# Kernel tuning notes

Hardware: AMD Instinct MI355X
Metric: run time of the kernel (lower is better)

The kernel has to match this reference:

```python
import jax, jax.numpy as jnp
import numpy as np

NA, NV, FEAT = 8000, 4000, 32
H, D = 4, 16            # heads, per-head dim
HD = H * D              # 64 node width
BLOCKS, DEPTH = 6, 2    # 12 attention layers total
OUT = 64
AK, AVK, VK = 10, 15, 15
EPS = 1e-5


def setup_inputs() -> dict:
    key = jax.random.key(0)
    ks = jax.random.split(key, 16)
    rn = lambda k, s, sc=0.1: (jax.random.normal(k, s, dtype=jnp.float32) * sc)
    return {
        "atom_x": rn(ks[0], (NA, FEAT), 1.0),
        "atom_pos": rn(ks[1], (NA, 3), 1.0),
        "vox_x": rn(ks[2], (NV, FEAT), 1.0),
        "vox_pos": rn(ks[3], (NV, 3), 1.0),
        "W_atom_in": rn(ks[4], (FEAT, HD)),
        "b_atom_in": jnp.zeros((HD,), jnp.float32),
        "W_vox_in": rn(ks[5], (FEAT, HD)),
        "b_vox_in": jnp.zeros((HD,), jnp.float32),
        "emlp_w1": rn(ks[6], (3, 1, 8), 0.5),
        "emlp_b1": jnp.zeros((3, 8), jnp.float32),
        "emlp_w2": rn(ks[7], (3, 8, 1), 0.5),
        "emlp_b2": jnp.zeros((3, 1), jnp.float32),
        "ln_g": jnp.ones((BLOCKS * DEPTH, HD), jnp.float32),
        "ln_b": jnp.zeros((BLOCKS * DEPTH, HD), jnp.float32),
        "Ws": rn(ks[8], (BLOCKS * DEPTH, HD, HD)),
        "Wd": rn(ks[9], (BLOCKS * DEPTH, HD, HD)),
        "We": rn(ks[10], (BLOCKS * DEPTH, 1, HD)),
        "att": rn(ks[11], (BLOCKS * DEPTH, H, D)),
        "Wo1": rn(ks[12], ((BLOCKS + 1) * HD, HD)),
        "bo1": jnp.zeros((HD,), jnp.float32),
        "Wo2": rn(ks[13], (HD, OUT)),
        "bo2": jnp.zeros((OUT,), jnp.float32),
    }


def _knn_edges(q_pos, c_pos, k, q_off, c_off):
    # for each query, k nearest candidates (single-graph batch)
    d2 = (jnp.sum(q_pos * q_pos, 1, keepdims=True)
          - 2.0 * q_pos @ c_pos.T
          + jnp.sum(c_pos * c_pos, 1))                      # [Nq, Nc]
    idx = jax.lax.top_k(-d2, k)[1]                          # [Nq, k]
    src = (idx + c_off).reshape(-1)
    dst = jnp.repeat(jnp.arange(q_pos.shape[0]) + q_off, k)
    return src, dst


def _forward(atom_x, atom_pos, vox_x, vox_pos,
             W_atom_in, b_atom_in, W_vox_in, b_vox_in,
             emlp_w1, emlp_b1, emlp_w2, emlp_b2,
             ln_g, ln_b, Ws, Wd, We, att, Wo1, bo1, Wo2, bo2):
    Na, Nv = atom_x.shape[0], vox_x.shape[0]
    N = Na + Nv
    x = jnp.concatenate([atom_x @ W_atom_in + b_atom_in,
                         vox_x @ W_vox_in + b_vox_in], 0)   # [N, HD]
    pos = jnp.concatenate([atom_pos, vox_pos], 0)           # [N, 3]

    # (query_pos, cand_pos, k, q_offset, c_offset, edge-MLP index)
    combos = [(atom_pos, atom_pos, AK, 0, 0, 0),    # atom<-atom
              (atom_pos, vox_pos, AVK, 0, Na, 1),   # atom<-vox
              (vox_pos, vox_pos, VK, Na, Na, 2)]    # vox<-vox
    srcs, dsts, attrs = [], [], []
    for qp, cp, k, qo, co, mi in combos:
        s, d = _knn_edges(qp, cp, k, qo, co)
        dist = jnp.linalg.norm(pos[s] - pos[d], axis=1, keepdims=True)  # [E,1]
        h = jax.nn.relu(dist @ emlp_w1[mi] + emlp_b1[mi])
        attrs.append(h @ emlp_w2[mi] + emlp_b2[mi])
        srcs.append(s); dsts.append(d)
    src = jnp.concatenate(srcs)
    dst = jnp.concatenate(dsts)
    eattr = jnp.concatenate(attrs, 0)                       # [E,1]

    def gat_layer(xin, l):
        mu = xin.mean(-1, keepdims=True)
        var = xin.var(-1, keepdims=True)
        h = (xin - mu) * jax.lax.rsqrt(var + EPS) * ln_g[l] + ln_b[l]
        s = (h @ Ws[l]).reshape(N, H, D)
        d_ = (h @ Wd[l]).reshape(N, H, D)
        e = (eattr @ We[l]).reshape(-1, H, D)
        m = s[src] + d_[dst] + e                            # [E,H,D]
        score = jnp.einsum('ehd,hd->eh', jax.nn.leaky_relu(m, 0.2), att[l])
        smax = jax.ops.segment_max(score, dst, num_segments=N)
        a = jnp.exp(score - smax[dst])
        denom = jax.ops.segment_sum(a, dst, num_segments=N)
        alpha = a / denom[dst]                              # softmax per dst node
        msg = jax.ops.segment_sum(alpha[..., None] * s[src], dst,
                                  num_segments=N).reshape(N, HD)
        return jax.nn.relu(xin + msg)

    outs = [x]
    cur = x
    for b in range(BLOCKS):
        for dd in range(DEPTH):
            cur = gat_layer(cur, b * DEPTH + dd)
        outs.append(cur)
    cat = jnp.concatenate(outs, -1)[Na:]                    # vox nodes, [Nv,448]
    enc = jax.nn.relu(cat @ Wo1 + bo1) @ Wo2 + bo2          # [Nv,OUT]
    return enc


def reference(atom_x, atom_pos, vox_x, vox_pos,
              W_atom_in, b_atom_in, W_vox_in, b_vox_in,
              emlp_w1, emlp_b1, emlp_w2, emlp_b2,
              ln_g, ln_b, Ws, Wd, We, att, Wo1, bo1, Wo2, bo2):
    enc = _forward(atom_x, atom_pos, vox_x, vox_pos,
                   W_atom_in, b_atom_in, W_vox_in, b_vox_in,
                   emlp_w1, emlp_b1, emlp_w2, emlp_b2,
                   ln_g, ln_b, Ws, Wd, We, att, Wo1, bo1, Wo2, bo2)
    return (enc, vox_pos)
```

## Files before the change

kernel.cpp:

```cpp
#include <hip/hip_runtime.h>
#include <math.h>

#define NA 8000
#define NV 4000
#define NN 12000
#define NA_PAD 8192
#define NV_PAD 4096
#define KNN_TILE 2048
#define FEAT 32
#define HD 64
#define NLAYER 12
#define E_AA 80000
#define E_AV 120000
#define E_VV 60000
#define E_TOT 260000
#define ENC_SIZE (NV * HD)
#define EPS 1e-5f

__device__ __forceinline__ float wave_sum64(float v) {
#pragma unroll
  for (int off = 1; off < 64; off <<= 1) v += __shfl_xor(v, off);
  return v;
}

__device__ __forceinline__ float dpp_step(float v, const int ctrl) {
  int p;
  switch (ctrl) {
    case 0xB1:  p = __builtin_amdgcn_update_dpp(0, __float_as_int(v), 0xB1,  0xF, 0xF, true); break;
    case 0x4E:  p = __builtin_amdgcn_update_dpp(0, __float_as_int(v), 0x4E,  0xF, 0xF, true); break;
    case 0x141: p = __builtin_amdgcn_update_dpp(0, __float_as_int(v), 0x141, 0xF, 0xF, true); break;
    default:    p = __builtin_amdgcn_update_dpp(0, __float_as_int(v), 0x140, 0xF, 0xF, true); break;
  }
  return v + __int_as_float(p);
}

__device__ __forceinline__ float head_sum16_dpp(float v) {
  v = dpp_step(v, 0xB1);
  v = dpp_step(v, 0x4E);
  v = dpp_step(v, 0x141);
  v = dpp_step(v, 0x140);
  return v;
}

__device__ __forceinline__ float wave_sum64_dpp(float v) {
  v = head_sum16_dpp(v);
  v += __shfl_xor(v, 16);
  v += __shfl_xor(v, 32);
  return v;
}

__global__ __launch_bounds__(256) void pack_kernel(
    const float* __restrict__ apos, const float* __restrict__ vpos,
    float4* __restrict__ apk, float4* __restrict__ vpk)
{
  const int i = blockIdx.x * 256 + threadIdx.x;
  if (i < NA_PAD) {
    float4 r;
    if (i < NA) {
      const float cx = apos[i*3+0], cy = apos[i*3+1], cz = apos[i*3+2];
      r = make_float4(cx, cy, cz, (cx*cx + cy*cy) + cz*cz);
    } else r = make_float4(0.f, 0.f, 0.f, INFINITY);
    apk[i] = r;
  } else {
    const int j = i - NA_PAD;
    if (j < NV_PAD) {
      float4 r;
      if (j < NV) {
        const float cx = vpos[j*3+0], cy = vpos[j*3+1], cz = vpos[j*3+2];
        r = make_float4(cx, cy, cz, (cx*cx + cy*cy) + cz*cz);
      } else r = make_float4(0.f, 0.f, 0.f, INFINITY);
      vpk[j] = r;
    }
  }
}

template<int K, int NC_PAD>
__device__ __attribute__((noinline)) void knn_body(
    const float* __restrict__ qpos, const float4* __restrict__ cpk,
    int c_off, int* __restrict__ out_src, int qblock)
{
  extern __shared__ float4 tile[];
  const int tid  = threadIdx.x;
  const int wid  = tid >> 6, lane = tid & 63;
  const int q    = qblock * 8 + wid;
  const float qx = qpos[q*3+0], qy = qpos[q*3+1], qz = qpos[q*3+2];
  const float qq = (qx*qx + qy*qy) + qz*qz;

  float eD = INFINITY; int eI = 0x7fffffff;
  float thrD = INFINITY;

  for (int t0 = 0; t0 < NC_PAD; t0 += KNN_TILE) {
    __syncthreads();
#pragma unroll
    for (int s = 0; s < KNN_TILE/512; ++s)
      tile[s*512 + tid] = cpk[t0 + s*512 + tid];
    __syncthreads();
#pragma unroll 8
    for (int it = 0; it < KNN_TILE/64; ++it) {
      const int j = t0 + it*64 + lane;
      const float4 c = tile[it*64 + lane];
      const float dot = qx*c.x + qy*c.y + qz*c.z;
      const float d2  = (qq - 2.0f*dot) + c.w;
      unsigned long long m = __ballot(d2 < thrD);
      if (m) {
        do {
          const int sl = __ffsll(m) - 1;
          m &= (m - 1ULL);
          const float v  = __shfl(d2, sl);
          const int   vi = j - lane + sl;
          const bool stay = (eD < v) || (eD == v && eI < vi);
          const float pD = __shfl_up(eD, 1);
          const int   pI = __shfl_up(eI, 1);
          int pS = __shfl_up(stay ? 1 : 0, 1);
          if (lane == 0) pS = 1;
          eD = stay ? eD : (pS ? v  : pD);
          eI = stay ? eI : (pS ? vi : pI);
        } while (m);
        thrD = __shfl(eD, K-1);
      }
    }
  }
  if (lane < K) out_src[q*K + lane] = eI + c_off;
}

__global__ __launch_bounds__(512) void knn_all_kernel(
    const float* __restrict__ apos, const float* __restrict__ vpos,
    const float4* __restrict__ apk, const float4* __restrict__ vpk,
    int* __restrict__ srcA, int* __restrict__ srcAV, int* __restrict__ srcVV)
{
  const int b = blockIdx.x;
  if (b < NA/8)
    knn_body<10, NA_PAD>(apos, apk, 0,  srcA,  b);
  else if (b < 2*(NA/8))
    knn_body<15, NV_PAD>(apos, vpk, NA, srcAV, b - NA/8);
  else
    knn_body<15, NV_PAD>(vpos, vpk, NA, srcVV, b - 2*(NA/8));
}

__device__ __forceinline__ void ln_sd(
    float v, int node, int lane, int l,
    const float* __restrict__ ln_g, const float* __restrict__ ln_b,
    const float* __restrict__ Ws, const float* __restrict__ Wd,
    float* __restrict__ sbuf, float* __restrict__ dbuf)
{
  const float m = wave_sum64_dpp(v) * (1.0f/64.0f);
  const float c = v - m;
  const float var = wave_sum64_dpp(c*c) * (1.0f/64.0f);
  const float hn = c * rsqrtf(var + EPS) * ln_g[l*HD + lane] + ln_b[l*HD + lane];
  const float* ws = Ws + (size_t)l*HD*HD;
  const float* wd = Wd + (size_t)l*HD*HD;
  float accs = 0.0f, accd = 0.0f;
#pragma unroll
  for (int j = 0; j < HD; ++j) {
    const float hj = __shfl(hn, j);
    accs += hj * ws[j*HD + lane];
    accd += hj * wd[j*HD + lane];
  }
  sbuf[node*HD + lane] = accs;
  dbuf[node*HD + lane] = accd;
}

__global__ __launch_bounds__(64) void init_kernel(
    const float* __restrict__ atom_x, const float* __restrict__ vox_x,
    const float* __restrict__ Wa, const float* __restrict__ ba,
    const float* __restrict__ Wv, const float* __restrict__ bv,
    const float* __restrict__ ln_g, const float* __restrict__ ln_b,
    const float* __restrict__ Ws, const float* __restrict__ Wd,
    float* __restrict__ x, float* __restrict__ snap0,
    float* __restrict__ sbuf, float* __restrict__ dbuf)
{
  const int node = blockIdx.x;
  const int t    = threadIdx.x;
  const float* in; const float* W; const float* b;
  if (node < NA) { in = atom_x + node*FEAT;     W = Wa; b = ba; }
  else           { in = vox_x + (node-NA)*FEAT; W = Wv; b = bv; }
  float acc = b[t];
#pragma unroll
  for (int j = 0; j < FEAT; ++j) acc += in[j] * W[j*HD + t];
  x[node*HD + t] = acc;
  if (node >= NA) snap0[(node-NA)*HD + t] = acc;
  ln_sd(acc, node, t, 0, ln_g, ln_b, Ws, Wd, sbuf, dbuf);
}

__device__ __forceinline__ void load_pos(const float* ap, const float* vp,
                                         int i, float& px, float& py, float& pz)
{
  const float* p = (i < NA) ? (ap + i*3) : (vp + (i - NA)*3);
  px = p[0]; py = p[1]; pz = p[2];
}

__global__ __launch_bounds__(256) void edge_attr_kernel(
    const float* __restrict__ atom_pos, const float* __restrict__ vox_pos,
    const int* __restrict__ srcA, const int* __restrict__ srcAV,
    const int* __restrict__ srcVV,
    const float* __restrict__ w1, const float* __restrict__ b1,
    const float* __restrict__ w2, const float* __restrict__ b2,
    float* __restrict__ eattr)
{
  const int e = blockIdx.x * 256 + threadIdx.x;
  if (e >= E_TOT) return;
  int s, d, mi;
  if (e < E_AA)              { mi = 0; s = srcA[e];                 d = e / 10; }
  else if (e < E_AA + E_AV)  { mi = 1; const int t = e - E_AA;      s = srcAV[t]; d = t / 15; }
  else                       { mi = 2; const int t = e - E_AA - E_AV; s = srcVV[t]; d = NA + t / 15; }
  float sx, sy, sz, dx_, dy_, dz_;
  load_pos(atom_pos, vox_pos, s, sx, sy, sz);
  load_pos(atom_pos, vox_pos, d, dx_, dy_, dz_);
  const float ex = sx - dx_, ey = sy - dy_, ez = sz - dz_;
  const float dist = sqrtf(ex*ex + ey*ey + ez*ez);
  float acc = b2[mi];
#pragma unroll
  for (int j = 0; j < 8; ++j) {
    float h = dist * w1[mi*8 + j] + b1[mi*8 + j];
    h = (h > 0.0f) ? h : 0.0f;
    acc += h * w2[mi*8 + j];
  }
  eattr[e] = acc;
}

template<int NE, bool IS_ATOM>
__device__ __forceinline__ float agg_node(
    int n, int lane,
    float* __restrict__ x,
    const float* __restrict__ sbuf, const float* __restrict__ dbuf,
    const float* __restrict__ eattr,
    const int* __restrict__ srcA, const int* __restrict__ srcAV,
    const int* __restrict__ srcVV,
    const float* __restrict__ We, const float* __restrict__ att, int l,
    float* __restrict__ snap)
{
  const float wet  = We[l*HD + lane];
  const float attv = att[l*HD + lane];
  const float dn   = dbuf[n*HD + lane];

  int esrc[NE]; float eat[NE];
#pragma unroll
  for (int e = 0; e < NE; ++e) {
    int src, eidx;
    if (IS_ATOM) {
      if (e < 10) { src = srcA[n*10 + e];       eidx = n*10 + e; }
      else        { src = srcAV[n*15 + (e-10)]; eidx = E_AA + n*15 + (e-10); }
    } else {
      const int nv = n - NA;
      src = srcVV[nv*15 + e]; eidx = E_AA + E_AV + nv*15 + e;
    }
    esrc[e] = src;
    eat[e]  = eattr[eidx];
  }

  float srow[NE];
#pragma unroll
  for (int e = 0; e < NE; ++e) srow[e] = sbuf[esrc[e]*HD + lane];

  float escore[NE];
#pragma unroll
  for (int e = 0; e < NE; ++e) {
    float mm = srow[e] + dn + eat[e] * wet;
    mm = (mm >= 0.0f) ? mm : 0.2f * mm;
    escore[e] = head_sum16_dpp(mm * attv);
  }
  float mx = -INFINITY;
#pragma unroll
  for (int e = 0; e < NE; ++e) mx = fmaxf(mx, escore[e]);
  float den = 0.0f;
#pragma unroll
  for (int e = 0; e < NE; ++e) {
    const float a = __expf(escore[e] - mx);
    escore[e] = a; den += a;
  }
  const float inv = 1.0f / den;
  float msg = 0.0f;
#pragma unroll
  for (int e = 0; e < NE; ++e) msg += (escore[e] * inv) * srow[e];
  float xv = x[n*HD + lane] + msg;
  xv = (xv > 0.0f) ? xv : 0.0f;
  x[n*HD + lane] = xv;
  if (!IS_ATOM && snap != nullptr) snap[(n - NA)*HD + lane] = xv;
  return xv;
}

__global__ __launch_bounds__(256, 4) void layer_kernel(
    float* __restrict__ x,
    const float* __restrict__ sbuf_in, float* __restrict__ dbuf,
    float* __restrict__ sbuf_out,
    const float* __restrict__ eattr,
    const int* __restrict__ srcA, const int* __restrict__ srcAV,
    const int* __restrict__ srcVV,
    const float* __restrict__ We, const float* __restrict__ att,
    const float* __restrict__ ln_g, const float* __restrict__ ln_b,
    const float* __restrict__ Ws, const float* __restrict__ Wd,
    int l, float* __restrict__ snap, int do_next)
{
  const int wid = threadIdx.x >> 6, lane = threadIdx.x & 63;
  const int n = blockIdx.x * 4 + wid;
  __shared__ float hn_sh[HD][4];
  __shared__ float part[4][4][2][HD];

  float xv;
  if (n < NA) {
    if (!do_next) return;
    xv = agg_node<25,true>(n, lane, x, sbuf_in, dbuf, eattr,
                           srcA, srcAV, srcVV, We, att, l, nullptr);
  } else {
    xv = agg_node<15,false>(n, lane, x, sbuf_in, dbuf, eattr,
                            srcA, srcAV, srcVV, We, att, l, snap);
  }
  if (!do_next) return;

  const int ln = l + 1;
  const float mean = wave_sum64_dpp(xv) * (1.0f/64.0f);
  const float cc   = xv - mean;
  const float var  = wave_sum64_dpp(cc*cc) * (1.0f/64.0f);
  const float hn   = cc * rsqrtf(var + EPS) * ln_g[ln*HD + lane] + ln_b[ln*HD + lane];
  hn_sh[lane][wid] = hn;
  __syncthreads();

  const float* wsp = Ws + (size_t)ln*HD*HD;
  const float* wdp = Wd + (size_t)ln*HD*HD;
  float as0=0.f, as1=0.f, as2=0.f, as3=0.f;
  float ad0=0.f, ad1=0.f, ad2=0.f, ad3=0.f;
#pragma unroll
  for (int jj = 0; jj < 16; ++jj) {
    const int j = wid*16 + jj;
    const float wvs = wsp[j*HD + lane];
    const float wvd = wdp[j*HD + lane];
    const float4 h = *(const float4*)&hn_sh[j][0];
    as0 += h.x*wvs; ad0 += h.x*wvd;
    as1 += h.y*wvs; ad1 += h.y*wvd;
    as2 += h.z*wvs; ad2 += h.z*wvd;
    as3 += h.w*wvs; ad3 += h.w*wvd;
  }
  part[wid][0][0][lane] = as0; part[wid][0][1][lane] = ad0;
  part[wid][1][0][lane] = as1; part[wid][1][1][lane] = ad1;
  part[wid][2][0][lane] = as2; part[wid][2][1][lane] = ad2;
  part[wid][3][0][lane] = as3; part[wid][3][1][lane] = ad3;
  __syncthreads();

  const float accs = ((part[0][wid][0][lane] + part[1][wid][0][lane])
                    + (part[2][wid][0][lane] + part[3][wid][0][lane]));
  const float accd = ((part[0][wid][1][lane] + part[1][wid][1][lane])
                    + (part[2][wid][1][lane] + part[3][wid][1][lane]));
  sbuf_out[n*HD + lane] = accs;
  dbuf[n*HD + lane]     = accd;
}

__global__ __launch_bounds__(256) void head_kernel(
    const float* __restrict__ snaps,
    const float* __restrict__ Wo1, const float* __restrict__ bo1,
    const float* __restrict__ Wo2, const float* __restrict__ bo2,
    float* __restrict__ out)
{
  const int wid = threadIdx.x >> 6, lane = threadIdx.x & 63;
  const int n = blockIdx.x * 4 + wid;
  __shared__ float cat[4][7*HD];
  __shared__ float part[4][4][HD];
  __shared__ float o1[4][HD];

#pragma unroll
  for (int c = 0; c < 7; ++c)
    cat[wid][c*HD + lane] = snaps[(size_t)c*NV*HD + n*HD + lane];
  __syncthreads();

  float a0=0.f, a1=0.f, a2=0.f, a3=0.f;
  for (int jj = 0; jj < 112; ++jj) {
    const int j = wid*112 + jj;
    const float w = Wo1[j*HD + lane];
    a0 += cat[0][j]*w; a1 += cat[1][j]*w;
    a2 += cat[2][j]*w; a3 += cat[3][j]*w;
  }
  part[wid][0][lane] = a0; part[wid][1][lane] = a1;
  part[wid][2][lane] = a2; part[wid][3][lane] = a3;
  __syncthreads();

  float acc = bo1[lane] + ((part[0][wid][lane] + part[1][wid][lane])
                         + (part[2][wid][lane] + part[3][wid][lane]));
  acc = fmaxf(acc, 0.0f);
  o1[wid][lane] = acc;
  __syncthreads();

  float b0=0.f, b1=0.f, b2=0.f, b3=0.f;
#pragma unroll
  for (int jj = 0; jj < 16; ++jj) {
    const int j = wid*16 + jj;
    const float w = Wo2[j*HD + lane];
    b0 += o1[0][j]*w; b1 += o1[1][j]*w;
    b2 += o1[2][j]*w; b3 += o1[3][j]*w;
  }
  __syncthreads();
  part[wid][0][lane] = b0; part[wid][1][lane] = b1;
  part[wid][2][lane] = b2; part[wid][3][lane] = b3;
  __syncthreads();

  const float acc2 = bo2[lane] + ((part[0][wid][lane] + part[1][wid][lane])
                                + (part[2][wid][lane] + part[3][wid][lane]));
  out[n*HD + lane] = acc2;
}

__global__ __launch_bounds__(256) void copy_pos_kernel(
    const float* __restrict__ vp, float* __restrict__ out)
{
  const int i = blockIdx.x * 256 + threadIdx.x;
  if (i < NV*3) out[ENC_SIZE + i] = vp[i];
}

extern "C" void kernel_launch(void* const* d_in, const int* in_sizes, int n_in,
                              void* d_out, int out_size, void* d_ws, size_t ws_size,
                              hipStream_t stream)
{
  const float* atom_x    = (const float*)d_in[0];
  const float* atom_pos  = (const float*)d_in[1];
  const float* vox_x     = (const float*)d_in[2];
  const float* vox_pos   = (const float*)d_in[3];
  const float* W_atom_in = (const float*)d_in[4];
  const float* b_atom_in = (const float*)d_in[5];
  const float* W_vox_in  = (const float*)d_in[6];
  const float* b_vox_in  = (const float*)d_in[7];
  const float* emlp_w1   = (const float*)d_in[8];
  const float* emlp_b1   = (const float*)d_in[9];
  const float* emlp_w2   = (const float*)d_in[10];
  const float* emlp_b2   = (const float*)d_in[11];
  const float* ln_g      = (const float*)d_in[12];
  const float* ln_b      = (const float*)d_in[13];
  const float* Ws        = (const float*)d_in[14];
  const float* Wd        = (const float*)d_in[15];
  const float* We        = (const float*)d_in[16];
  const float* att       = (const float*)d_in[17];
  const float* Wo1       = (const float*)d_in[18];
  const float* bo1       = (const float*)d_in[19];
  const float* Wo2       = (const float*)d_in[20];
  const float* bo2       = (const float*)d_in[21];
  float* out = (float*)d_out;

  float* ws    = (float*)d_ws;
  float* x     = ws;
  float* sA    = x  + (size_t)NN*HD;
  float* sB    = sA + (size_t)NN*HD;
  float* dbuf  = sB + (size_t)NN*HD;
  float* eattr = dbuf + (size_t)NN*HD;
  float* snaps = eattr + E_TOT;
  int*   srcA  = (int*)(snaps + (size_t)7*NV*HD);
  int*   srcAV = srcA  + E_AA;
  int*   srcVV = srcAV + E_AV;
  float4* apk  = (float4*)(srcVV + E_VV);
  float4* vpk  = apk + NA_PAD;

  pack_kernel<<<(NA_PAD + NV_PAD + 255)/256, 256, 0, stream>>>(
      atom_pos, vox_pos, apk, vpk);
  knn_all_kernel<<<NA/8 + NA/8 + NV/8, 512, KNN_TILE*sizeof(float4), stream>>>(
      atom_pos, vox_pos, apk, vpk, srcA, srcAV, srcVV);
  edge_attr_kernel<<<(E_TOT + 255)/256, 256, 0, stream>>>(
      atom_pos, vox_pos, srcA, srcAV, srcVV,
      emlp_w1, emlp_b1, emlp_w2, emlp_b2, eattr);
  init_kernel<<<NN, 64, 0, stream>>>(atom_x, vox_x, W_atom_in, b_atom_in,
                                     W_vox_in, b_vox_in, ln_g, ln_b, Ws, Wd,
                                     x, snaps, sA, dbuf);
  for (int l = 0; l < NLAYER; ++l) {
    float* s_in  = (l & 1) ? sB : sA;
    float* s_out = (l & 1) ? sA : sB;
    float* snap  = (l & 1) ? (snaps + (size_t)(l/2 + 1)*NV*HD) : nullptr;
    layer_kernel<<<NN/4, 256, 0, stream>>>(x, s_in, dbuf, s_out, eattr,
                                           srcA, srcAV, srcVV, We, att,
                                           ln_g, ln_b, Ws, Wd, l, snap,
                                           (l < NLAYER-1) ? 1 : 0);
  }
  head_kernel<<<NV/4, 256, 0, stream>>>(snaps, Wo1, bo1, Wo2, bo2, out);
  copy_pos_kernel<<<(NV*3 + 255)/256, 256, 0, stream>>>(vox_pos, out);
}
```

Measured before the change: 392.4 us.

## Fuse the twelve GAT layer launches into one persistent cooperative kernel

Moves the per-layer body into a device function and adds a persistent cooperative kernel. It loops over all layers with a grid-stride loop over 4-node groups and a grid-wide sync between layers, replacing twelve separate launches. The aim is to remove per-launch overhead and the idle tail between layer kernels. The grid size is the occupancy query result times a hardcoded 256 CUs, and the old per-layer launches remain as a fallback if the cooperative launch fails. Grid-wide barriers add their own cost, and the grid-stride loop gives each block several groups per layer.

Result: slower. 1.553 ms (+295.7%).

```diff
diff --git a/kernel.cpp b/kernel.cpp
--- a/kernel.cpp
+++ b/kernel.cpp
@@ -1,4 +1,5 @@
 #include <hip/hip_runtime.h>
+#include <hip/hip_cooperative_groups.h>
 #include <math.h>
 
 #define NA 8000
@@ -16,6 +17,7 @@
 #define E_TOT 260000
 #define ENC_SIZE (NV * HD)
 #define EPS 1e-5f
+#define NGRP (NN/4)
 
 __device__ __forceinline__ float wave_sum64(float v) {
 #pragma unroll
@@ -279,6 +281,69 @@
   return xv;
 }
 
+__device__ __forceinline__ void layer_group(
+    int g, int wid, int lane,
+    float* __restrict__ x,
+    const float* __restrict__ sbuf_in, float* __restrict__ dbuf,
+    float* __restrict__ sbuf_out,
+    const float* __restrict__ eattr,
+    const int* __restrict__ srcA, const int* __restrict__ srcAV,
+    const int* __restrict__ srcVV,
+    const float* __restrict__ We, const float* __restrict__ att,
+    const float* __restrict__ ln_g, const float* __restrict__ ln_b,
+    const float* __restrict__ Ws, const float* __restrict__ Wd,
+    int l, float* __restrict__ snap, int do_next,
+    float (*hn_sh)[4], float (*part)[4][2][HD])
+{
+  const int n = g * 4 + wid;
+  float xv;
+  if (n < NA) {
+    if (!do_next) return;
+    xv = agg_node<25,true>(n, lane, x, sbuf_in, dbuf, eattr,
+                           srcA, srcAV, srcVV, We, att, l, nullptr);
+  } else {
+    xv = agg_node<15,false>(n, lane, x, sbuf_in, dbuf, eattr,
+                            srcA, srcAV, srcVV, We, att, l, snap);
+  }
+  if (!do_next) return;
+
+  const int ln = l + 1;
+  const float mean = wave_sum64_dpp(xv) * (1.0f/64.0f);
+  const float cc   = xv - mean;
+  const float var  = wave_sum64_dpp(cc*cc) * (1.0f/64.0f);
+  const float hn   = cc * rsqrtf(var + EPS) * ln_g[ln*HD + lane] + ln_b[ln*HD + lane];
+  hn_sh[lane][wid] = hn;
+  __syncthreads();
+
+  const float* wsp = Ws + (size_t)ln*HD*HD;
+  const float* wdp = Wd + (size_t)ln*HD*HD;
+  float as0=0.f, as1=0.f, as2=0.f, as3=0.f;
+  float ad0=0.f, ad1=0.f, ad2=0.f, ad3=0.f;
+#pragma unroll
+  for (int jj = 0; jj < 16; ++jj) {
+    const int j = wid*16 + jj;
+    const float wvs = wsp[j*HD + lane];
+    const float wvd = wdp[j*HD + lane];
+    const float4 h = *(const float4*)&hn_sh[j][0];
+    as0 += h.x*wvs; ad0 += h.x*wvd;
+    as1 += h.y*wvs; ad1 += h.y*wvd;
+    as2 += h.z*wvs; ad2 += h.z*wvd;
+    as3 += h.w*wvs; ad3 += h.w*wvd;
+  }
+  part[wid][0][0][lane] = as0; part[wid][0][1][lane] = ad0;
+  part[wid][1][0][lane] = as1; part[wid][1][1][lane] = ad1;
+  part[wid][2][0][lane] = as2; part[wid][2][1][lane] = ad2;
+  part[wid][3][0][lane] = as3; part[wid][3][1][lane] = ad3;
+  __syncthreads();
+
+  const float accs = ((part[0][wid][0][lane] + part[1][wid][0][lane])
+                    + (part[2][wid][0][lane] + part[3][wid][0][lane]));
+  const float accd = ((part[0][wid][1][lane] + part[1][wid][1][lane])
+                    + (part[2][wid][1][lane] + part[3][wid][1][lane]));
+  sbuf_out[n*HD + lane] = accs;
+  dbuf[n*HD + lane]     = accd;
+}
+
 __global__ __launch_bounds__(256, 4) void layer_kernel(
     float* __restrict__ x,
     const float* __restrict__ sbuf_in, float* __restrict__ dbuf,
@@ -292,56 +357,40 @@
     int l, float* __restrict__ snap, int do_next)
 {
   const int wid = threadIdx.x >> 6, lane = threadIdx.x & 63;
-  const int n = blockIdx.x * 4 + wid;
   __shared__ float hn_sh[HD][4];
   __shared__ float part[4][4][2][HD];
-
-  float xv;
-  if (n < NA) {
-    if (!do_next) return;
-    xv = agg_node<25,true>(n, lane, x, sbuf_in, dbuf, eattr,
-                           srcA, srcAV, srcVV, We, att, l, nullptr);
-  } else {
-    xv = agg_node<15,false>(n, lane, x, sbuf_in, dbuf, eattr,
-                            srcA, srcAV, srcVV, We, att, l, snap);
-  }
-  if (!do_next) return;
-
-  const int ln = l + 1;
-  const float mean = wave_sum64_dpp(xv) * (1.0f/64.0f);
-  const float cc   = xv - mean;
-  const float var  = wave_sum64_dpp(cc*cc) * (1.0f/64.0f);
-  const float hn   = cc * rsqrtf(var + EPS) * ln_g[ln*HD + lane] + ln_b[ln*HD + lane];
-  hn_sh[lane][wid] = hn;
-  __syncthreads();
-
-  const float* wsp = Ws + (size_t)ln*HD*HD;
-  const float* wdp = Wd + (size_t)ln*HD*HD;
-  float as0=0.f, as1=0.f, as2=0.f, as3=0.f;
-  float ad0=0.f, ad1=0.f, ad2=0.f, ad3=0.f;
-#pragma unroll
-  for (int jj = 0; jj < 16; ++jj) {
-    const int j = wid*16 + jj;
-    const float wvs = wsp[j*HD + lane];
-    const float wvd = wdp[j*HD + lane];
-    const float4 h = *(const float4*)&hn_sh[j][0];
-    as0 += h.x*wvs; ad0 += h.x*wvd;
-    as1 += h.y*wvs; ad1 += h.y*wvd;
-    as2 += h.z*wvs; ad2 += h.z*wvd;
-    as3 += h.w*wvs; ad3 += h.w*wvd;
-  }
-  part[wid][0][0][lane] = as0; part[wid][0][1][lane] = ad0;
-  part[wid][1][0][lane] = as1; part[wid][1][1][lane] = ad1;
-  part[wid][2][0][lane] = as2; part[wid][2][1][lane] = ad2;
-  part[wid][3][0][lane] = as3; part[wid][3][1][lane] = ad3;
-  __syncthreads();
-
-  const float accs = ((part[0][wid][0][lane] + part[1][wid][0][lane])
-                    + (part[2][wid][0][lane] + part[3][wid][0][lane]));
-  const float accd = ((part[0][wid][1][lane] + part[1][wid][1][lane])
-                    + (part[2][wid][1][lane] + part[3][wid][1][lane]));
-  sbuf_out[n*HD + lane] = accs;
-  dbuf[n*HD + lane]     = accd;
+  layer_group(blockIdx.x, wid, lane, x, sbuf_in, dbuf, sbuf_out, eattr,
+              srcA, srcAV, srcVV, We, att, ln_g, ln_b, Ws, Wd,
+              l, snap, do_next, hn_sh, part);
+}
+
+__global__ __launch_bounds__(256, 4) void layers_all_kernel(
+    float* __restrict__ x, float* __restrict__ sA, float* __restrict__ sB,
+    float* __restrict__ dbuf, const float* __restrict__ eattr,
+    const int* __restrict__ srcA, const int* __restrict__ srcAV,
+    const int* __restrict__ srcVV,
+    const float* __restrict__ We, const float* __restrict__ att,
+    const float* __restrict__ ln_g, const float* __restrict__ ln_b,
+    const float* __restrict__ Ws, const float* __restrict__ Wd,
+    float* __restrict__ snaps)
+{
+  cooperative_groups::grid_group grid = cooperative_groups::this_grid();
+  const int wid = threadIdx.x >> 6, lane = threadIdx.x & 63;
+  __shared__ float hn_sh[HD][4];
+  __shared__ float part[4][4][2][HD];
+
+  for (int l = 0; l < NLAYER; ++l) {
+    const float* sbuf_in  = (l & 1) ? sB : sA;
+    float*       sbuf_out = (l & 1) ? sA : sB;
+    float* snap = (l & 1) ? (snaps + (size_t)(l/2 + 1)*NV*HD) : nullptr;
+    const int do_next = (l < NLAYER-1) ? 1 : 0;
+    for (int g = blockIdx.x; g < NGRP; g += gridDim.x) {
+      layer_group(g, wid, lane, x, sbuf_in, dbuf, sbuf_out, eattr,
+                  srcA, srcAV, srcVV, We, att, ln_g, ln_b, Ws, Wd,
+                  l, snap, do_next, hn_sh, part);
+    }
+    grid.sync();
+  }
 }
 
 __global__ __launch_bounds__(256) void head_kernel(
@@ -454,14 +503,36 @@
   init_kernel<<<NN, 64, 0, stream>>>(atom_x, vox_x, W_atom_in, b_atom_in,
                                      W_vox_in, b_vox_in, ln_g, ln_b, Ws, Wd,
                                      x, snaps, sA, dbuf);
-  for (int l = 0; l < NLAYER; ++l) {
-    float* s_in  = (l & 1) ? sB : sA;
-    float* s_out = (l & 1) ? sA : sB;
-    float* snap  = (l & 1) ? (snaps + (size_t)(l/2 + 1)*NV*HD) : nullptr;
-    layer_kernel<<<NN/4, 256, 0, stream>>>(x, s_in, dbuf, s_out, eattr,
-                                           srcA, srcAV, srcVV, We, att,
-                                           ln_g, ln_b, Ws, Wd, l, snap,
-                                           (l < NLAYER-1) ? 1 : 0);
+  bool coop_done = false;
+  {
+    int maxb = 0;
+    hipError_t qerr = hipOccupancyMaxActiveBlocksPerMultiprocessor(
+        &maxb, layers_all_kernel, 256, 0);
+    int nblocks = (qerr == hipSuccess) ? maxb * 256 : 0;
+    if (nblocks > NGRP) nblocks = NGRP;
+    if (nblocks >= 256) {
+      void* cargs[] = {
+        (void*)&x, (void*)&sA, (void*)&sB, (void*)&dbuf, (void*)&eattr,
+        (void*)&srcA, (void*)&srcAV, (void*)&srcVV,
+        (void*)&We, (void*)&att, (void*)&ln_g, (void*)&ln_b,
+        (void*)&Ws, (void*)&Wd, (void*)&snaps
+      };
+      hipError_t lerr = hipLaunchCooperativeKernel(
+          (const void*)layers_all_kernel, dim3(nblocks), dim3(256),
+          cargs, 0, stream);
+      coop_done = (lerr == hipSuccess);
+    }
+  }
+  if (!coop_done) {
+    for (int l = 0; l < NLAYER; ++l) {
+      float* s_in  = (l & 1) ? sB : sA;
+      float* s_out = (l & 1) ? sA : sB;
+      float* snap  = (l & 1) ? (snaps + (size_t)(l/2 + 1)*NV*HD) : nullptr;
+      layer_kernel<<<NGRP, 256, 0, stream>>>(x, s_in, dbuf, s_out, eattr,
+                                             srcA, srcAV, srcVV, We, att,
+                                             ln_g, ln_b, Ws, Wd, l, snap,
+                                             (l < NLAYER-1) ? 1 : 0);
+    }
   }
   head_kernel<<<NV/4, 256, 0, stream>>>(snaps, Wo1, bo1, Wo2, bo2, out);
   copy_pos_kernel<<<(NV*3 + 255)/256, 256, 0, stream>>>(vox_pos, out);
```
